# Kernel tuning notes

Measured on AMD Instinct MI355X. Metric: run time of the kernel, lower is better.

The kernel has to match this reference:

```python
import jax, jax.numpy as jnp
import numpy as np

N = 100000
E = 1600000
F_IN = 128
HID = 64
N_CLASS = 40
NEG_SLOPE = 0.2


def setup_inputs() -> dict:
    key = jax.random.key(0)
    ks = jax.random.split(key, 16)
    s = lambda *sh: 1.0 / np.sqrt(sh[0])
    inp = {
        "x": jax.random.normal(ks[0], (N, F_IN), dtype=jnp.float32),
        "edge_index": jax.random.randint(ks[1], (2, E), 0, N, dtype=jnp.int64),
        "W1": jax.random.normal(ks[2], (F_IN, HID), jnp.float32) * s(F_IN),
        "b1": jnp.zeros((HID,), jnp.float32),
        "Wc0": jax.random.normal(ks[3], (HID, HID), jnp.float32) * s(HID),
        "att_src0": jax.random.normal(ks[4], (HID,), jnp.float32) * s(HID),
        "att_dst0": jax.random.normal(ks[5], (HID,), jnp.float32) * s(HID),
        "bias0": jnp.zeros((HID,), jnp.float32),
        "Wc1": jax.random.normal(ks[6], (HID, HID), jnp.float32) * s(HID),
        "att_src1": jax.random.normal(ks[7], (HID,), jnp.float32) * s(HID),
        "att_dst1": jax.random.normal(ks[8], (HID,), jnp.float32) * s(HID),
        "bias1": jnp.zeros((HID,), jnp.float32),
        "W2": jax.random.normal(ks[9], (HID, N_CLASS), jnp.float32) * s(HID),
        "b2": jnp.zeros((N_CLASS,), jnp.float32),
    }
    return inp


def gat_conv(x, src, dst, W, att_src, att_dst, bias):
    # x: [N, Fin]; src/dst: [E'] (self-loops already appended)
    h = x @ W                                   # [N, Fout]
    a_s = h @ att_src                           # [N]
    a_d = h @ att_dst                           # [N]
    e = jax.nn.leaky_relu(a_s[src] + a_d[dst], NEG_SLOPE)   # [E']
    # segment softmax over edges grouped by destination node
    e_max = jax.ops.segment_max(e, dst, num_segments=N)     # every node has a self-loop
    ex = jnp.exp(e - e_max[dst])
    denom = jax.ops.segment_sum(ex, dst, num_segments=N)
    alpha = ex / (denom[dst] + 1e-16)                        # [E']
    out = jax.ops.segment_sum(h[src] * alpha[:, None], dst, num_segments=N)
    return out + bias


def reference(x, edge_index, W1, b1, Wc0, att_src0, att_dst0, bias0,
              Wc1, att_src1, att_dst1, bias1, W2, b2):
    # eval mode: dropout_adj and feature dropout are identity
    loop = jnp.arange(N, dtype=edge_index.dtype)
    src = jnp.concatenate([edge_index[0], loop])
    dst = jnp.concatenate([edge_index[1], loop])

    h = jax.nn.relu(x @ W1 + b1)
    h = gat_conv(h, src, dst, Wc0, att_src0, att_dst0, bias0)
    h = jax.nn.relu(h)
    h = gat_conv(h, src, dst, Wc1, att_src1, att_dst1, bias1)
    logits = h @ W2 + b2
    return jax.nn.log_softmax(logits, axis=-1)
```

## Files before the change

kernel.cpp:

```cpp
#include <hip/hip_runtime.h>

#define N_NODES 100000
#define N_EDGES 1600000
#define F_IN    128
#define HID     64
#define N_CLASS 40
#define NEG_SLOPE 0.2f
#define ET (N_EDGES + N_NODES)
#define ROW_BLOCKS ((N_NODES + 63) / 64)

#define NCB   7
#define CAP1  294912
#define BPC   144
#define NFB   782
#define CAPF  2624
#define NT1   ((ET + 2047) / 2048)

typedef __attribute__((ext_vector_type(8))) short bf16x8;
typedef __attribute__((ext_vector_type(4))) float f32x4;

__device__ __forceinline__ unsigned int f2bf(float f) {
    unsigned int u = __float_as_uint(f);
    return (u + 0x7fffu + ((u >> 16) & 1u)) >> 16;
}

__global__ __launch_bounds__(256) void k_prepw(const float* __restrict__ W1,
        const float* __restrict__ Wc0, const float* __restrict__ Wc1,
        const float* __restrict__ W2,
        unsigned short* __restrict__ Wt1, unsigned short* __restrict__ Wtc0,
        unsigned short* __restrict__ Wtc1, unsigned short* __restrict__ W2t,
        int* __restrict__ zbuf, int zcount) {
    int t = threadIdx.x;
    for (int i = t; i < zcount; i += 256) zbuf[i] = 0;
    for (int i = t; i < F_IN * HID; i += 256) {
        int k = i >> 6, n = i & 63;
        Wt1[n * F_IN + k] = (unsigned short)f2bf(W1[i]);
    }
    for (int i = t; i < HID * HID; i += 256) {
        int k = i >> 6, n = i & 63;
        Wtc0[n * HID + k] = (unsigned short)f2bf(Wc0[i]);
        Wtc1[n * HID + k] = (unsigned short)f2bf(Wc1[i]);
    }
    for (int i = t; i < 48 * HID; i += 256) {
        int n = i >> 6, k = i & 63;
        W2t[n * HID + k] = (n < N_CLASS)
            ? (unsigned short)f2bf(W2[k * N_CLASS + n]) : (unsigned short)0;
    }
}

__global__ __launch_bounds__(256) void k_lin1att(const float* __restrict__ x,
        const unsigned short* __restrict__ Wt1, const float* __restrict__ b1,
        const unsigned short* __restrict__ Wtc0,
        const float* __restrict__ att_s, const float* __restrict__ att_d,
        unsigned short* __restrict__ hb, float* __restrict__ as_,
        float* __restrict__ ad_) {
    __shared__ float xs[4][16 * 68];
    int t = threadIdx.x;
    int lane = t & 63, w = t >> 6;
    int quad = lane >> 4, lr = lane & 15;
    int rowg0 = blockIdx.x * 64 + w * 16;

    f32x4 zero = {0.f, 0.f, 0.f, 0.f};
    f32x4 acc[4] = {zero, zero, zero, zero};
    int arow = rowg0 + lr; if (arow >= N_NODES) arow = N_NODES - 1;
    const float* ab = x + (size_t)arow * F_IN;
    #pragma unroll
    for (int kc = 0; kc < 4; ++kc) {
        bf16x8 bw[4];
        #pragma unroll
        for (int nt = 0; nt < 4; ++nt)
            bw[nt] = *(const bf16x8*)(Wt1 + (nt * 16 + lr) * F_IN
                                      + kc * 32 + quad * 8);
        const float* ap = ab + kc * 32 + quad * 8;
        float4 a0 = *(const float4*)ap;
        float4 a1 = *(const float4*)(ap + 4);
        union { bf16x8 v; unsigned int u[4]; } af;
        af.u[0] = f2bf(a0.x) | (f2bf(a0.y) << 16);
        af.u[1] = f2bf(a0.z) | (f2bf(a0.w) << 16);
        af.u[2] = f2bf(a1.x) | (f2bf(a1.y) << 16);
        af.u[3] = f2bf(a1.z) | (f2bf(a1.w) << 16);
        #pragma unroll
        for (int nt = 0; nt < 4; ++nt)
            acc[nt] = __builtin_amdgcn_mfma_f32_16x16x32_bf16(
                          af.v, bw[nt], acc[nt], 0, 0, 0);
    }
    #pragma unroll
    for (int nt = 0; nt < 4; ++nt) {
        float bv = b1[nt * 16 + lr];
        #pragma unroll
        for (int reg = 0; reg < 4; ++reg)
            xs[w][(quad * 4 + reg) * 68 + nt * 16 + lr] =
                fmaxf(acc[nt][reg] + bv, 0.f);
    }
    f32x4 acc2[4] = {zero, zero, zero, zero};
    #pragma unroll
    for (int kc = 0; kc < 2; ++kc) {
        bf16x8 bw[4];
        #pragma unroll
        for (int nt = 0; nt < 4; ++nt)
            bw[nt] = *(const bf16x8*)(Wtc0 + (nt * 16 + lr) * HID
                                      + kc * 32 + quad * 8);
        const float* ap = xs[w] + lr * 68 + kc * 32 + quad * 8;
        float4 a0 = *(const float4*)ap;
        float4 a1 = *(const float4*)(ap + 4);
        union { bf16x8 v; unsigned int u[4]; } af;
        af.u[0] = f2bf(a0.x) | (f2bf(a0.y) << 16);
        af.u[1] = f2bf(a0.z) | (f2bf(a0.w) << 16);
        af.u[2] = f2bf(a1.x) | (f2bf(a1.y) << 16);
        af.u[3] = f2bf(a1.z) | (f2bf(a1.w) << 16);
        #pragma unroll
        for (int nt = 0; nt < 4; ++nt)
            acc2[nt] = __builtin_amdgcn_mfma_f32_16x16x32_bf16(
                          af.v, bw[nt], acc2[nt], 0, 0, 0);
    }
    float asv[4], adv[4];
    #pragma unroll
    for (int nt = 0; nt < 4; ++nt) {
        asv[nt] = att_s[nt * 16 + lr];
        adv[nt] = att_d[nt * 16 + lr];
    }
    #pragma unroll
    for (int reg = 0; reg < 4; ++reg) {
        float p1 = acc2[0][reg] * asv[0] + acc2[1][reg] * asv[1]
                 + acc2[2][reg] * asv[2] + acc2[3][reg] * asv[3];
        float p2 = acc2[0][reg] * adv[0] + acc2[1][reg] * adv[1]
                 + acc2[2][reg] * adv[2] + acc2[3][reg] * adv[3];
        #pragma unroll
        for (int off = 1; off < 16; off <<= 1) {
            p1 += __shfl_xor(p1, off, 64);
            p2 += __shfl_xor(p2, off, 64);
        }
        if (lr == 0) {
            int grow = rowg0 + quad * 4 + reg;
            if (grow < N_NODES) { as_[grow] = p1; ad_[grow] = p2; }
        }
    }
    #pragma unroll
    for (int nt = 0; nt < 4; ++nt)
        #pragma unroll
        for (int reg = 0; reg < 4; ++reg)
            xs[w][(quad * 4 + reg) * 68 + nt * 16 + lr] = acc2[nt][reg];
    #pragma unroll
    for (int j = 0; j < 2; ++j) {
        int task = j * 64 + lane;
        int r = task >> 3, g = task & 7;
        int grow = rowg0 + r;
        if (grow < N_NODES) {
            const float* p = xs[w] + r * 68 + g * 8;
            uint4 u;
            u.x = f2bf(p[0]) | (f2bf(p[1]) << 16);
            u.y = f2bf(p[2]) | (f2bf(p[3]) << 16);
            u.z = f2bf(p[4]) | (f2bf(p[5]) << 16);
            u.w = f2bf(p[6]) | (f2bf(p[7]) << 16);
            *(uint4*)(hb + (size_t)grow * HID + g * 8) = u;
        }
    }
}

__global__ __launch_bounds__(256) void k_gemm_att(
        const unsigned short* __restrict__ hin,
        const unsigned short* __restrict__ Wt,
        const float* __restrict__ att_s, const float* __restrict__ att_d,
        unsigned short* __restrict__ hb, float* __restrict__ as_,
        float* __restrict__ ad_) {
    __shared__ float xs[4][16 * 68];
    int t = threadIdx.x;
    int lane = t & 63, w = t >> 6;
    int quad = lane >> 4, lr = lane & 15;
    int rowg0 = blockIdx.x * 64 + w * 16;

    bf16x8 bfr[2][4];
    #pragma unroll
    for (int kc = 0; kc < 2; ++kc)
        #pragma unroll
        for (int nt = 0; nt < 4; ++nt)
            bfr[kc][nt] = *(const bf16x8*)(Wt + (nt * 16 + lr) * HID
                                           + kc * 32 + quad * 8);
    f32x4 zero = {0.f, 0.f, 0.f, 0.f};
    f32x4 acc[4] = {zero, zero, zero, zero};

    int arow = rowg0 + lr; if (arow >= N_NODES) arow = N_NODES - 1;
    #pragma unroll
    for (int kc = 0; kc < 2; ++kc) {
        bf16x8 af = *(const bf16x8*)(hin + (size_t)arow * HID
                                     + kc * 32 + quad * 8);
        #pragma unroll
        for (int nt = 0; nt < 4; ++nt)
            acc[nt] = __builtin_amdgcn_mfma_f32_16x16x32_bf16(
                          af, bfr[kc][nt], acc[nt], 0, 0, 0);
    }
    float asv[4], adv[4];
    #pragma unroll
    for (int nt = 0; nt < 4; ++nt) {
        asv[nt] = att_s[nt * 16 + lr];
        adv[nt] = att_d[nt * 16 + lr];
    }
    #pragma unroll
    for (int reg = 0; reg < 4; ++reg) {
        float p1 = acc[0][reg] * asv[0] + acc[1][reg] * asv[1]
                 + acc[2][reg] * asv[2] + acc[3][reg] * asv[3];
        float p2 = acc[0][reg] * adv[0] + acc[1][reg] * adv[1]
                 + acc[2][reg] * adv[2] + acc[3][reg] * adv[3];
        #pragma unroll
        for (int off = 1; off < 16; off <<= 1) {
            p1 += __shfl_xor(p1, off, 64);
            p2 += __shfl_xor(p2, off, 64);
        }
        if (lr == 0) {
            int grow = rowg0 + quad * 4 + reg;
            if (grow < N_NODES) { as_[grow] = p1; ad_[grow] = p2; }
        }
    }
    #pragma unroll
    for (int nt = 0; nt < 4; ++nt)
        #pragma unroll
        for (int reg = 0; reg < 4; ++reg)
            xs[w][(quad * 4 + reg) * 68 + nt * 16 + lr] = acc[nt][reg];
    #pragma unroll
    for (int j = 0; j < 2; ++j) {
        int task = j * 64 + lane;
        int r = task >> 3, g = task & 7;
        int grow = rowg0 + r;
        if (grow < N_NODES) {
            const float* p = xs[w] + r * 68 + g * 8;
            uint4 u;
            u.x = f2bf(p[0]) | (f2bf(p[1]) << 16);
            u.y = f2bf(p[2]) | (f2bf(p[3]) << 16);
            u.z = f2bf(p[4]) | (f2bf(p[5]) << 16);
            u.w = f2bf(p[6]) | (f2bf(p[7]) << 16);
            *(uint4*)(hb + (size_t)grow * HID + g * 8) = u;
        }
    }
}

__global__ __launch_bounds__(256) void k_part1(const int* __restrict__ ei,
        int* __restrict__ tail1, int2* __restrict__ buf1) {
    __shared__ int2 eb[2048];
    __shared__ int hist[NCB], lbase[NCB], loff[NCB], goff[NCB];
    int t = threadIdx.x;
    int tileBase = blockIdx.x * 2048;
    int total = ET - tileBase; if (total > 2048) total = 2048;
    if (t < NCB) hist[t] = 0;
    __syncthreads();

    int sr[8], dr[8];
    #pragma unroll
    for (int r = 0; r < 8; ++r) {
        int i = tileBase + r * 256 + t;
        int s = -1, d = -1;
        if (i < ET) {
            if (i < N_EDGES) { s = ei[i]; d = ei[N_EDGES + i]; }
            else             { s = d = i - N_EDGES; }
            atomicAdd(&hist[d >> 14], 1);
        }
        sr[r] = s; dr[r] = d;
    }
    __syncthreads();
    if (t == 0) {
        int run = 0;
        for (int b = 0; b < NCB; ++b) { lbase[b] = run; loff[b] = 0; run += hist[b]; }
    }
    __syncthreads();
    if (t < NCB && hist[t] > 0) goff[t] = atomicAdd(&tail1[t], hist[t]);
    #pragma unroll
    for (int r = 0; r < 8; ++r) {
        if (dr[r] >= 0) {
            int b = dr[r] >> 14;
            int p = lbase[b] + atomicAdd(&loff[b], 1);
            eb[p] = make_int2(sr[r], dr[r]);
        }
    }
    __syncthreads();
    for (int j = t; j < total; j += 256) {
        int2 e = eb[j];
        int b = e.y >> 14;
        buf1[(size_t)b * CAP1 + goff[b] + (j - lbase[b])] = e;
    }
}

__global__ __launch_bounds__(256) void k_part2(const int2* __restrict__ buf1,
        const int* __restrict__ tail1, int* __restrict__ fcnt,
        int2* __restrict__ buf2) {
    __shared__ int2 eb[2048];
    __shared__ int hist[128], lbase[128], loff[128], goff[128], sc[128];
    int t = threadIdx.x;
    int cb   = blockIdx.x / BPC;
    int tile = blockIdx.x % BPC;
    int n1 = tail1[cb];
    int base = tile * 2048;
    if (base >= n1) return;
    int total = n1 - base; if (total > 2048) total = 2048;
    if (t < 128) hist[t] = 0;
    __syncthreads();

    int sr[8], dr[8];
    #pragma unroll
    for (int r = 0; r < 8; ++r) {
        int i = base + r * 256 + t;
        int s = -1, d = -1;
        if (i < n1) {
            int2 e = buf1[(size_t)cb * CAP1 + i];
            s = e.x; d = e.y;
            atomicAdd(&hist[(d >> 7) & 127], 1);
        }
        sr[r] = s; dr[r] = d;
    }
    __syncthreads();
    if (t < 128) sc[t] = hist[t];
    __syncthreads();
    for (int off = 1; off < 128; off <<= 1) {
        int u = (t < 128 && t >= off) ? sc[t - off] : 0;
        __syncthreads();
        if (t < 128) sc[t] += u;
        __syncthreads();
    }
    if (t < 128) { lbase[t] = sc[t] - hist[t]; loff[t] = 0; }
    __syncthreads();
    if (t < 128 && hist[t] > 0)
        goff[t] = atomicAdd(&fcnt[cb * 128 + t], hist[t]);
    #pragma unroll
    for (int r = 0; r < 8; ++r) {
        if (dr[r] >= 0) {
            int f = (dr[r] >> 7) & 127;
            int p = lbase[f] + atomicAdd(&loff[f], 1);
            eb[p] = make_int2(sr[r], dr[r]);
        }
    }
    __syncthreads();
    for (int j = t; j < total; j += 256) {
        int2 e = eb[j];
        int f = (e.y >> 7) & 127;
        buf2[(size_t)(e.y >> 7) * CAPF + goff[f] + (j - lbase[f])] = e;
    }
}

__global__ __launch_bounds__(1024) void k_fscan(const int* __restrict__ fcnt,
        int* __restrict__ fbase, int* __restrict__ rowptr) {
    __shared__ int s[1024];
    int t = threadIdx.x;
    int v = (t < NFB) ? fcnt[t] : 0;
    s[t] = v;
    __syncthreads();
    for (int off = 1; off < 1024; off <<= 1) {
        int u = (t >= off) ? s[t - off] : 0;
        __syncthreads();
        s[t] += u;
        __syncthreads();
    }
    if (t < NFB) fbase[t] = s[t] - v;
    if (t == 0) rowptr[N_NODES] = ET;
}

__global__ __launch_bounds__(256) void k_part3(const int2* __restrict__ buf2,
        const int* __restrict__ fcnt, const int* __restrict__ fbase,
        int* __restrict__ rowptr, int* __restrict__ col,
        int* __restrict__ dhistg) {
    __shared__ int2 eb[CAPF];
    __shared__ int cs[CAPF];
    __shared__ int hist[128], lbase[128], loff[128], sc[128], dh[64];
    int t = threadIdx.x;
    int fb = blockIdx.x;
    int nF = fcnt[fb];
    int gb = fbase[fb];
    int nbase = fb * 128;
    if (t < 128) hist[t] = 0;
    if (t >= 128 && t < 192) dh[t - 128] = 0;
    __syncthreads();
    for (int j = t; j < nF; j += 256) {
        int2 e = buf2[(size_t)fb * CAPF + j];
        eb[j] = e;
        atomicAdd(&hist[e.y - nbase], 1);
    }
    __syncthreads();
    if (t < 128) sc[t] = hist[t];
    __syncthreads();
    for (int off = 1; off < 128; off <<= 1) {
        int u = (t < 128 && t >= off) ? sc[t - off] : 0;
        __syncthreads();
        if (t < 128) sc[t] += u;
        __syncthreads();
    }
    if (t < 128) { lbase[t] = sc[t] - hist[t]; loff[t] = 0; }
    __syncthreads();
    if (t < 128 && nbase + t < N_NODES) {
        rowptr[nbase + t] = gb + lbase[t];
        int dg = hist[t]; if (dg > 63) dg = 63;
        atomicAdd(&dh[dg], 1);
    }
    for (int j = t; j < nF; j += 256) {
        int2 e = eb[j];
        int r = e.y - nbase;
        int p = lbase[r] + atomicAdd(&loff[r], 1);
        cs[p] = e.x;
    }
    __syncthreads();
    for (int j = t; j < nF; j += 256) col[gb + j] = cs[j];
    if (t < 64 && dh[t] > 0) atomicAdd(&dhistg[t], dh[t]);
}

__global__ __launch_bounds__(64) void k_dscan(const int* __restrict__ dhist,
        int* __restrict__ dbase) {
    int t = threadIdx.x;
    int v = dhist[t];
    int s = v;
    #pragma unroll
    for (int off = 1; off < 64; off <<= 1) {
        int u = __shfl_up(s, off, 64);
        if (t >= off) s += u;
    }
    dbase[t] = s - v;
}

__global__ __launch_bounds__(256) void k_dscatter(const int* __restrict__ rowptr,
        int* __restrict__ dbase, int* __restrict__ nodeord) {
    __shared__ int lh[64], goff[64];
    int t = threadIdx.x;
    if (t < 64) lh[t] = 0;
    __syncthreads();
    int i = blockIdx.x * 256 + t;
    int deg = -1, lrank = 0;
    if (i < N_NODES) {
        deg = rowptr[i + 1] - rowptr[i];
        if (deg > 63) deg = 63;
        lrank = atomicAdd(&lh[deg], 1);
    }
    __syncthreads();
    if (t < 64) goff[t] = (lh[t] > 0) ? atomicAdd(&dbase[t], lh[t]) : 0;
    __syncthreads();
    if (deg >= 0) nodeord[goff[deg] + lrank] = i;
}

template <bool RELU>
__global__ __launch_bounds__(256) void k_gat_agg(const int* __restrict__ rowptr,
        const int* __restrict__ col, const unsigned short* __restrict__ hb,
        const float* __restrict__ as_, const float* __restrict__ ad_,
        const float* __restrict__ bias, const int* __restrict__ nodeord,
        unsigned short* __restrict__ outb) {
    int t = threadIdx.x;
    int lane = t & 63;
    int wid = blockIdx.x * 4 + (t >> 6);
    int l8 = lane & 7;
    int ch = l8 * 8;
    int d = nodeord[wid * 8 + (lane >> 3)];
    int beg = rowptr[d];
    int deg = rowptr[d + 1] - beg;
    float add = ad_[d];
    int degw = deg;
    degw = max(degw, __shfl_xor(degw, 8, 64));
    degw = max(degw, __shfl_xor(degw, 16, 64));
    degw = max(degw, __shfl_xor(degw, 32, 64));

    float a0=0.f,a1=0.f,a2=0.f,a3=0.f,a4=0.f,a5=0.f,a6=0.f,a7=0.f,den=0.f;
    const unsigned short* hch = hb + ch;
    for (int c = 0; c < degw; c += 8) {
        int idx = c + l8;
        int sj = 0; float wj = 0.f;
        if (idx < deg) {
            sj = col[beg + idx];
            float e = as_[sj] + add;
            e = (e > 0.f) ? e : NEG_SLOPE * e;
            wj = __expf(e);
        }
        #pragma unroll
        for (int j = 0; j < 8; ++j) {
            int sl = (lane & 56) | j;
            int   s  = __shfl(sj, sl, 64);
            float w0 = __shfl(wj, sl, 64);
            den += w0;
            uint4 hv = *(const uint4*)(hch + (size_t)s * HID);
            a0 = fmaf(w0, __uint_as_float(hv.x << 16),         a0);
            a1 = fmaf(w0, __uint_as_float(hv.x & 0xffff0000u), a1);
            a2 = fmaf(w0, __uint_as_float(hv.y << 16),         a2);
            a3 = fmaf(w0, __uint_as_float(hv.y & 0xffff0000u), a3);
            a4 = fmaf(w0, __uint_as_float(hv.z << 16),         a4);
            a5 = fmaf(w0, __uint_as_float(hv.z & 0xffff0000u), a5);
            a6 = fmaf(w0, __uint_as_float(hv.w << 16),         a6);
            a7 = fmaf(w0, __uint_as_float(hv.w & 0xffff0000u), a7);
        }
    }
    float inv = 1.f / (den + 1e-16f);
    float4 bA = *(const float4*)(bias + ch);
    float4 bB = *(const float4*)(bias + ch + 4);
    float o0 = fmaf(a0, inv, bA.x), o1 = fmaf(a1, inv, bA.y);
    float o2 = fmaf(a2, inv, bA.z), o3 = fmaf(a3, inv, bA.w);
    float o4 = fmaf(a4, inv, bB.x), o5 = fmaf(a5, inv, bB.y);
    float o6 = fmaf(a6, inv, bB.z), o7 = fmaf(a7, inv, bB.w);
    if (RELU) {
        o0 = fmaxf(o0, 0.f); o1 = fmaxf(o1, 0.f);
        o2 = fmaxf(o2, 0.f); o3 = fmaxf(o3, 0.f);
        o4 = fmaxf(o4, 0.f); o5 = fmaxf(o5, 0.f);
        o6 = fmaxf(o6, 0.f); o7 = fmaxf(o7, 0.f);
    }
    uint4 u;
    u.x = f2bf(o0) | (f2bf(o1) << 16);
    u.y = f2bf(o2) | (f2bf(o3) << 16);
    u.z = f2bf(o4) | (f2bf(o5) << 16);
    u.w = f2bf(o6) | (f2bf(o7) << 16);
    *(uint4*)(outb + (size_t)d * HID + ch) = u;
}

__global__ __launch_bounds__(256) void k_final(
        const unsigned short* __restrict__ aggb,
        const unsigned short* __restrict__ W2t, const float* __restrict__ b2,
        float* __restrict__ out) {
    __shared__ float xs[64 * 44];
    int t = threadIdx.x;
    int lane = t & 63, w = t >> 6;
    int quad = lane >> 4, lr = lane & 15;
    int rowg0 = blockIdx.x * 64 + w * 16;
    int base = blockIdx.x * 64;
    int rem = N_NODES - base; if (rem > 64) rem = 64;

    bf16x8 bfr[2][3];
    #pragma unroll
    for (int kc = 0; kc < 2; ++kc)
        #pragma unroll
        for (int nt = 0; nt < 3; ++nt)
            bfr[kc][nt] = *(const bf16x8*)(W2t + (nt * 16 + lr) * HID
                                           + kc * 32 + quad * 8);
    f32x4 zero = {0.f, 0.f, 0.f, 0.f};
    f32x4 acc[3] = {zero, zero, zero};
    int arow = rowg0 + lr; if (arow >= N_NODES) arow = N_NODES - 1;
    #pragma unroll
    for (int kc = 0; kc < 2; ++kc) {
        bf16x8 af = *(const bf16x8*)(aggb + (size_t)arow * HID
                                     + kc * 32 + quad * 8);
        #pragma unroll
        for (int nt = 0; nt < 3; ++nt)
            acc[nt] = __builtin_amdgcn_mfma_f32_16x16x32_bf16(
                          af, bfr[kc][nt], acc[nt], 0, 0, 0);
    }
    float bc[3];
    #pragma unroll
    for (int nt = 0; nt < 3; ++nt) {
        int cl = nt * 16 + lr;
        bc[nt] = (cl < N_CLASS) ? b2[cl] : -1e30f;
    }
    #pragma unroll
    for (int reg = 0; reg < 4; ++reg) {
        float v0 = acc[0][reg] + bc[0];
        float v1 = acc[1][reg] + bc[1];
        float v2 = acc[2][reg] + bc[2];
        float m = fmaxf(fmaxf(v0, v1), v2);
        #pragma unroll
        for (int off = 1; off < 16; off <<= 1)
            m = fmaxf(m, __shfl_xor(m, off, 64));
        float ss = __expf(v0 - m) + __expf(v1 - m) + __expf(v2 - m);
        #pragma unroll
        for (int off = 1; off < 16; off <<= 1)
            ss += __shfl_xor(ss, off, 64);
        float lse = m + logf(ss);
        int r = w * 16 + quad * 4 + reg;
        xs[r * 44 + lr]      = v0 - lse;
        xs[r * 44 + 16 + lr] = v1 - lse;
        if (lr < 8) xs[r * 44 + 32 + lr] = v2 - lse;
    }
    __syncthreads();
    #pragma unroll
    for (int j = 0; j < 3; ++j) {
        int idx = j * 256 + t;
        if (idx < rem * 10) {
            int r = idx / 10, c4 = idx - r * 10;
            float4 v = *(const float4*)(xs + r * 44 + c4 * 4);
            *(float4*)(out + (size_t)base * N_CLASS + idx * 4) = v;
        }
    }
}

extern "C" void kernel_launch(void* const* d_in, const int* in_sizes, int n_in,
                              void* d_out, int out_size, void* d_ws, size_t ws_size,
                              hipStream_t stream) {
    const float* x     = (const float*)d_in[0];
    const int*   ei    = (const int*)  d_in[1];
    const float* W1    = (const float*)d_in[2];
    const float* b1    = (const float*)d_in[3];
    const float* Wc0   = (const float*)d_in[4];
    const float* as0   = (const float*)d_in[5];
    const float* ad0   = (const float*)d_in[6];
    const float* bias0 = (const float*)d_in[7];
    const float* Wc1   = (const float*)d_in[8];
    const float* as1   = (const float*)d_in[9];
    const float* ad1   = (const float*)d_in[10];
    const float* bias1 = (const float*)d_in[11];
    const float* W2    = (const float*)d_in[12];
    const float* b2    = (const float*)d_in[13];
    float* out = (float*)d_out;

    char* basep = (char*)d_ws;
    char* R1 = basep;
    char* R2 = basep + (size_t)N_NODES * HID * 4;
    unsigned short* agg1b = (unsigned short*)R1;
    int*            nodeord = (int*)(R1 + (size_t)N_NODES * HID * 2);
    int2*           buf2  = (int2*)R1;
    unsigned short* hb    = (unsigned short*)R2;
    unsigned short* agg0b = (unsigned short*)(R2 + (size_t)N_NODES * HID * 2);
    int2*           buf1  = (int2*)R2;

    char* mp = R2 + (size_t)N_NODES * HID * 4;
    unsigned short* Wt1  = (unsigned short*)mp;  mp += F_IN * HID * 2;
    unsigned short* Wtc0 = (unsigned short*)mp;  mp += HID * HID * 2;
    unsigned short* Wtc1 = (unsigned short*)mp;  mp += HID * HID * 2;
    unsigned short* W2t  = (unsigned short*)mp;  mp += 48 * HID * 2;
    float* as_   = (float*)mp;                   mp += N_NODES * 4;
    float* ad_   = (float*)mp;                   mp += N_NODES * 4;
    int*   col   = (int*)mp;                     mp += (size_t)ET * 4;
    int*   tail1 = (int*)mp;                     mp += NCB * 4;
    int*   fcnt  = (int*)mp;                     mp += NFB * 4;
    int*   fbase = (int*)mp;                     mp += NFB * 4;
    int*   dhist = (int*)mp;                     mp += 64 * 4;
    int*   dbase = (int*)mp;                     mp += 64 * 4;
    int*   rowptr= (int*)mp;
    const int ZCOUNT = NCB + 2 * NFB + 128;

    const int AGG_BLOCKS = N_NODES / 32;
    const int NODE_BLOCKS = (N_NODES + 255) / 256;

    k_prepw<<<1, 256, 0, stream>>>(W1, Wc0, Wc1, W2, Wt1, Wtc0, Wtc1, W2t,
                                   tail1, ZCOUNT);
    k_part1<<<NT1, 256, 0, stream>>>(ei, tail1, buf1);
    k_part2<<<NCB * BPC, 256, 0, stream>>>(buf1, tail1, fcnt, buf2);
    k_fscan<<<1, 1024, 0, stream>>>(fcnt, fbase, rowptr);
    k_part3<<<NFB, 256, 0, stream>>>(buf2, fcnt, fbase, rowptr, col, dhist);
    k_dscan<<<1, 64, 0, stream>>>(dhist, dbase);
    k_dscatter<<<NODE_BLOCKS, 256, 0, stream>>>(rowptr, dbase, nodeord);

    k_lin1att<<<ROW_BLOCKS, 256, 0, stream>>>(x, Wt1, b1, Wtc0, as0, ad0,
                                              hb, as_, ad_);
    k_gat_agg<true><<<AGG_BLOCKS, 256, 0, stream>>>(
        rowptr, col, hb, as_, ad_, bias0, nodeord, agg0b);

    k_gemm_att<<<ROW_BLOCKS, 256, 0, stream>>>(agg0b, Wtc1, as1, ad1,
                                               hb, as_, ad_);
    k_gat_agg<false><<<AGG_BLOCKS, 256, 0, stream>>>(
        rowptr, col, hb, as_, ad_, bias1, nodeord, agg1b);

    k_final<<<ROW_BLOCKS, 256, 0, stream>>>(agg1b, W2t, b2, out);
}
```

Measured before the change: 312.9 us.

## Fuse edge partition pass with first linear layer and fold scans into last blocks

Merges the first edge-partition pass and the input linear/attention kernel into one launch, with blocks split by index, so the two independent stages can overlap on the GPU. Edge records are packed into 32-bit words (source shifted left, low destination bits) instead of int2 pairs, halving the partition buffer traffic. The separate single-block scan kernels are removed: the last-finishing block of part2 and part3, detected with an atomic counter, does the scan. The weight prep kernel now runs on 32 blocks, and the workspace layout is reorganized, adding completion counters and some risk from the packed-index bit widths.

```diff
diff --git a/kernel.cpp b/kernel.cpp
--- a/kernel.cpp
+++ b/kernel.cpp
@@ -30,27 +30,378 @@
         unsigned short* __restrict__ Wt1, unsigned short* __restrict__ Wtc0,
         unsigned short* __restrict__ Wtc1, unsigned short* __restrict__ W2t,
         int* __restrict__ zbuf, int zcount) {
-    int t = threadIdx.x;
-    for (int i = t; i < zcount; i += 256) zbuf[i] = 0;
-    for (int i = t; i < F_IN * HID; i += 256) {
+    int g = blockIdx.x * 256 + threadIdx.x;
+    int stride = gridDim.x * 256;
+    for (int i = g; i < zcount; i += stride) zbuf[i] = 0;
+    for (int i = g; i < F_IN * HID; i += stride) {
         int k = i >> 6, n = i & 63;
         Wt1[n * F_IN + k] = (unsigned short)f2bf(W1[i]);
     }
-    for (int i = t; i < HID * HID; i += 256) {
+    for (int i = g; i < HID * HID; i += stride) {
         int k = i >> 6, n = i & 63;
         Wtc0[n * HID + k] = (unsigned short)f2bf(Wc0[i]);
         Wtc1[n * HID + k] = (unsigned short)f2bf(Wc1[i]);
     }
-    for (int i = t; i < 48 * HID; i += 256) {
+    for (int i = g; i < 48 * HID; i += stride) {
         int n = i >> 6, k = i & 63;
         W2t[n * HID + k] = (n < N_CLASS)
             ? (unsigned short)f2bf(W2[k * N_CLASS + n]) : (unsigned short)0;
     }
 }
 
-__global__ __launch_bounds__(256) void k_lin1att(const float* __restrict__ x,
-        const unsigned short* __restrict__ Wt1, const float* __restrict__ b1,
-        const unsigned short* __restrict__ Wtc0,
+__global__ __launch_bounds__(256) void k_p1lin(
+        const int* __restrict__ ei, int* __restrict__ tail1,
+        unsigned int* __restrict__ buf1,
+        const float* __restrict__ x, const unsigned short* __restrict__ Wt1,
+        const float* __restrict__ b1, const unsigned short* __restrict__ Wtc0,
+        const float* __restrict__ att_s, const float* __restrict__ att_d,
+        unsigned short* __restrict__ hb, float* __restrict__ as_,
+        float* __restrict__ ad_) {
+    __shared__ __align__(16) char smem[17408];
+    __shared__ int hist[NCB], lb[NCB], cbase[NCB];
+    int t = threadIdx.x;
+    int lane = t & 63, w = t >> 6;
+
+    if (blockIdx.x < NT1) {
+        unsigned int* eb = (unsigned int*)smem;
+        int tileBase = blockIdx.x * 2048;
+        int total = ET - tileBase; if (total > 2048) total = 2048;
+        if (t < NCB) hist[t] = 0;
+        __syncthreads();
+        unsigned long long ltm = (1ull << lane) - 1ull;
+        unsigned int pk[8]; int ps[8];
+        #pragma unroll
+        for (int r = 0; r < 8; ++r) {
+            int i = tileBase + r * 256 + t;
+            int s = 0, d = 0;
+            bool valid = (i < ET);
+            if (valid) {
+                if (i < N_EDGES) { s = ei[i]; d = ei[N_EDGES + i]; }
+                else             { s = d = i - N_EDGES; }
+            }
+            int b = valid ? (d >> 14) : -1;
+            unsigned long long m[NCB];
+            #pragma unroll
+            for (int q = 0; q < NCB; ++q) m[q] = __ballot(b == q);
+            int cnt = 0;
+            #pragma unroll
+            for (int q = 0; q < NCB; ++q) if (lane == q) cnt = __popcll(m[q]);
+            int old = 0;
+            if (lane < NCB) old = atomicAdd(&hist[lane], cnt);
+            int bsafe = valid ? b : 0;
+            int basew = __shfl(old, bsafe, 64);
+            if (valid) {
+                int rank = 0;
+                #pragma unroll
+                for (int q = 0; q < NCB; ++q)
+                    if (b == q) rank = (int)__popcll(m[q] & ltm);
+                pk[r] = ((unsigned int)s << 14) | ((unsigned int)d & 16383u);
+                ps[r] = (basew + rank) | (b << 12);
+            } else ps[r] = -1;
+        }
+        __syncthreads();
+        if (t == 0) {
+            int run = 0;
+            #pragma unroll
+            for (int q = 0; q < NCB; ++q) { int h = hist[q]; lb[q] = run; run += h; }
+        }
+        __syncthreads();
+        if (t < NCB) {
+            int g = (hist[t] > 0) ? atomicAdd(&tail1[t], hist[t]) : 0;
+            cbase[t] = g - lb[t];
+        }
+        #pragma unroll
+        for (int r = 0; r < 8; ++r) {
+            if (ps[r] >= 0) {
+                int b = ps[r] >> 12, pos = ps[r] & 4095;
+                eb[lb[b] + pos] = pk[r];
+            }
+        }
+        __syncthreads();
+        int B1 = lb[1], B2 = lb[2], B3 = lb[3], B4 = lb[4], B5 = lb[5], B6 = lb[6];
+        for (int j = t; j < total; j += 256) {
+            unsigned int p = eb[j];
+            int b = (j >= B1) + (j >= B2) + (j >= B3) + (j >= B4)
+                  + (j >= B5) + (j >= B6);
+            buf1[(size_t)b * CAP1 + cbase[b] + j] = p;
+        }
+    } else {
+        int quad = lane >> 4, lr = lane & 15;
+        int rowg0 = (int)(blockIdx.x - NT1) * 64 + w * 16;
+        float* xs = (float*)smem + w * (16 * 68);
+
+        f32x4 zero = {0.f, 0.f, 0.f, 0.f};
+        f32x4 acc[4] = {zero, zero, zero, zero};
+        int arow = rowg0 + lr; if (arow >= N_NODES) arow = N_NODES - 1;
+        const float* ab = x + (size_t)arow * F_IN;
+        #pragma unroll
+        for (int kc = 0; kc < 4; ++kc) {
+            bf16x8 bw[4];
+            #pragma unroll
+            for (int nt = 0; nt < 4; ++nt)
+                bw[nt] = *(const bf16x8*)(Wt1 + (nt * 16 + lr) * F_IN
+                                          + kc * 32 + quad * 8);
+            const float* ap = ab + kc * 32 + quad * 8;
+            float4 a0 = *(const float4*)ap;
+            float4 a1 = *(const float4*)(ap + 4);
+            union { bf16x8 v; unsigned int u[4]; } af;
+            af.u[0] = f2bf(a0.x) | (f2bf(a0.y) << 16);
+            af.u[1] = f2bf(a0.z) | (f2bf(a0.w) << 16);
+            af.u[2] = f2bf(a1.x) | (f2bf(a1.y) << 16);
+            af.u[3] = f2bf(a1.z) | (f2bf(a1.w) << 16);
+            #pragma unroll
+            for (int nt = 0; nt < 4; ++nt)
+                acc[nt] = __builtin_amdgcn_mfma_f32_16x16x32_bf16(
+                              af.v, bw[nt], acc[nt], 0, 0, 0);
+        }
+        #pragma unroll
+        for (int nt = 0; nt < 4; ++nt) {
+            float bv = b1[nt * 16 + lr];
+            #pragma unroll
+            for (int reg = 0; reg < 4; ++reg)
+                xs[(quad * 4 + reg) * 68 + nt * 16 + lr] =
+                    fmaxf(acc[nt][reg] + bv, 0.f);
+        }
+        f32x4 acc2[4] = {zero, zero, zero, zero};
+        #pragma unroll
+        for (int kc = 0; kc < 2; ++kc) {
+            bf16x8 bw[4];
+            #pragma unroll
+            for (int nt = 0; nt < 4; ++nt)
+                bw[nt] = *(const bf16x8*)(Wtc0 + (nt * 16 + lr) * HID
+                                          + kc * 32 + quad * 8);
+            const float* ap = xs + lr * 68 + kc * 32 + quad * 8;
+            float4 a0 = *(const float4*)ap;
+            float4 a1 = *(const float4*)(ap + 4);
+            union { bf16x8 v; unsigned int u[4]; } af;
+            af.u[0] = f2bf(a0.x) | (f2bf(a0.y) << 16);
+            af.u[1] = f2bf(a0.z) | (f2bf(a0.w) << 16);
+            af.u[2] = f2bf(a1.x) | (f2bf(a1.y) << 16);
+            af.u[3] = f2bf(a1.z) | (f2bf(a1.w) << 16);
+            #pragma unroll
+            for (int nt = 0; nt < 4; ++nt)
+                acc2[nt] = __builtin_amdgcn_mfma_f32_16x16x32_bf16(
+                              af.v, bw[nt], acc2[nt], 0, 0, 0);
+        }
+        float asv[4], adv[4];
+        #pragma unroll
+        for (int nt = 0; nt < 4; ++nt) {
+            asv[nt] = att_s[nt * 16 + lr];
+            adv[nt] = att_d[nt * 16 + lr];
+        }
+        #pragma unroll
+        for (int reg = 0; reg < 4; ++reg) {
+            float p1 = acc2[0][reg] * asv[0] + acc2[1][reg] * asv[1]
+                     + acc2[2][reg] * asv[2] + acc2[3][reg] * asv[3];
+            float p2 = acc2[0][reg] * adv[0] + acc2[1][reg] * adv[1]
+                     + acc2[2][reg] * adv[2] + acc2[3][reg] * adv[3];
+            #pragma unroll
+            for (int off = 1; off < 16; off <<= 1) {
+                p1 += __shfl_xor(p1, off, 64);
+                p2 += __shfl_xor(p2, off, 64);
+            }
+            if (lr == 0) {
+                int grow = rowg0 + quad * 4 + reg;
+                if (grow < N_NODES) { as_[grow] = p1; ad_[grow] = p2; }
+            }
+        }
+        #pragma unroll
+        for (int nt = 0; nt < 4; ++nt)
+            #pragma unroll
+            for (int reg = 0; reg < 4; ++reg)
+                xs[(quad * 4 + reg) * 68 + nt * 16 + lr] = acc2[nt][reg];
+        #pragma unroll
+        for (int j = 0; j < 2; ++j) {
+            int task = j * 64 + lane;
+            int r = task >> 3, g = task & 7;
+            int grow = rowg0 + r;
+            if (grow < N_NODES) {
+                const float* p = xs + r * 68 + g * 8;
+                uint4 u;
+                u.x = f2bf(p[0]) | (f2bf(p[1]) << 16);
+                u.y = f2bf(p[2]) | (f2bf(p[3]) << 16);
+                u.z = f2bf(p[4]) | (f2bf(p[5]) << 16);
+                u.w = f2bf(p[6]) | (f2bf(p[7]) << 16);
+                *(uint4*)(hb + (size_t)grow * HID + g * 8) = u;
+            }
+        }
+    }
+}
+
+__global__ __launch_bounds__(256) void k_part2(const unsigned int* __restrict__ buf1,
+        const int* __restrict__ tail1, int* __restrict__ fcnt,
+        unsigned int* __restrict__ buf2, int* __restrict__ fbase,
+        int* __restrict__ rowptr, int* __restrict__ done0) {
+    __shared__ unsigned int eb[2048];
+    __shared__ int hist[128], lbase[128], loff[128], goff[128], sc[128];
+    __shared__ int lastflag, wsum4[4];
+    int t = threadIdx.x;
+    int cb   = blockIdx.x / BPC;
+    int tile = blockIdx.x % BPC;
+    int n1 = tail1[cb];
+    int base = tile * 2048;
+    if (base < n1) {
+        int total = n1 - base; if (total > 2048) total = 2048;
+        if (t < 128) hist[t] = 0;
+        __syncthreads();
+        unsigned int pr[8]; int fr[8];
+        #pragma unroll
+        for (int r = 0; r < 8; ++r) {
+            int i = base + r * 256 + t;
+            int f = -1; unsigned int p = 0;
+            if (i < n1) {
+                p = buf1[(size_t)cb * CAP1 + i];
+                f = (int)((p >> 7) & 127u);
+                atomicAdd(&hist[f], 1);
+            }
+            pr[r] = p; fr[r] = f;
+        }
+        __syncthreads();
+        if (t < 128) sc[t] = hist[t];
+        __syncthreads();
+        for (int off = 1; off < 128; off <<= 1) {
+            int u = (t < 128 && t >= off) ? sc[t - off] : 0;
+            __syncthreads();
+            if (t < 128) sc[t] += u;
+            __syncthreads();
+        }
+        if (t < 128) { lbase[t] = sc[t] - hist[t]; loff[t] = 0; }
+        __syncthreads();
+        if (t < 128 && hist[t] > 0)
+            goff[t] = atomicAdd(&fcnt[cb * 128 + t], hist[t]);
+        #pragma unroll
+        for (int r = 0; r < 8; ++r) {
+            if (fr[r] >= 0) {
+                int f = fr[r];
+                int pos = lbase[f] + atomicAdd(&loff[f], 1);
+                eb[pos] = (pr[r] & 127u) | ((pr[r] >> 14) << 7)
+                        | ((unsigned int)f << 24);
+            }
+        }
+        __syncthreads();
+        for (int j = t; j < total; j += 256) {
+            unsigned int q = eb[j];
+            int f = (int)(q >> 24);
+            buf2[(size_t)(cb * 128 + f) * CAPF + goff[f] + (j - lbase[f])] =
+                q & 0xFFFFFFu;
+        }
+    }
+    if (t == 0) lastflag = (atomicAdd(done0, 1) == NCB * BPC - 1);
+    __syncthreads();
+    if (lastflag) {
+        __threadfence();
+        int k0 = t * 4;
+        int v0 = (k0     < NFB) ? fcnt[k0]     : 0;
+        int v1 = (k0 + 1 < NFB) ? fcnt[k0 + 1] : 0;
+        int v2 = (k0 + 2 < NFB) ? fcnt[k0 + 2] : 0;
+        int v3 = (k0 + 3 < NFB) ? fcnt[k0 + 3] : 0;
+        int s1 = v0 + v1, s2 = s1 + v2, s3 = s2 + v3;
+        int lane = t & 63, w = t >> 6;
+        int ws = s3;
+        #pragma unroll
+        for (int off = 1; off < 64; off <<= 1) {
+            int u = __shfl_up(ws, off, 64);
+            if (lane >= off) ws += u;
+        }
+        if (lane == 63) wsum4[w] = ws;
+        __syncthreads();
+        int wb = 0;
+        #pragma unroll
+        for (int q = 0; q < 4; ++q) if (q < w) wb += wsum4[q];
+        int ex = wb + ws - s3;
+        if (k0     < NFB) fbase[k0]     = ex;
+        if (k0 + 1 < NFB) fbase[k0 + 1] = ex + v0;
+        if (k0 + 2 < NFB) fbase[k0 + 2] = ex + s1;
+        if (k0 + 3 < NFB) fbase[k0 + 3] = ex + s2;
+        if (t == 0) rowptr[N_NODES] = ET;
+    }
+}
+
+__global__ __launch_bounds__(256) void k_part3(const unsigned int* __restrict__ buf2,
+        const int* __restrict__ fcnt, const int* __restrict__ fbase,
+        int* __restrict__ rowptr, int* __restrict__ col,
+        int* __restrict__ dhistg, int* __restrict__ dbase,
+        int* __restrict__ done1) {
+    __shared__ unsigned int eb[CAPF];
+    __shared__ int cs[CAPF];
+    __shared__ int hist[128], lbase[128], loff[128], sc[128], dh[64];
+    __shared__ int lastflag;
+    int t = threadIdx.x;
+    int fb = blockIdx.x;
+    int nF = fcnt[fb];
+    int gb = fbase[fb];
+    int nbase = fb * 128;
+    if (t < 128) hist[t] = 0;
+    if (t >= 128 && t < 192) dh[t - 128] = 0;
+    __syncthreads();
+    for (int j = t; j < nF; j += 256) {
+        unsigned int q = buf2[(size_t)fb * CAPF + j];
+        eb[j] = q;
+        atomicAdd(&hist[q & 127u], 1);
+    }
+    __syncthreads();
+    if (t < 128) sc[t] = hist[t];
+    __syncthreads();
+    for (int off = 1; off < 128; off <<= 1) {
+        int u = (t < 128 && t >= off) ? sc[t - off] : 0;
+        __syncthreads();
+        if (t < 128) sc[t] += u;
+        __syncthreads();
+    }
+    if (t < 128) { lbase[t] = sc[t] - hist[t]; loff[t] = 0; }
+    __syncthreads();
+    if (t < 128 && nbase + t < N_NODES) {
+        rowptr[nbase + t] = gb + lbase[t];
+        int dg = hist[t]; if (dg > 63) dg = 63;
+        atomicAdd(&dh[dg], 1);
+    }
+    for (int j = t; j < nF; j += 256) {
+        unsigned int q = eb[j];
+        int r = (int)(q & 127u);
+        int p = lbase[r] + atomicAdd(&loff[r], 1);
+        cs[p] = (int)(q >> 7);
+    }
+    __syncthreads();
+    for (int j = t; j < nF; j += 256) col[gb + j] = cs[j];
+    if (t < 64 && dh[t] > 0) atomicAdd(&dhistg[t], dh[t]);
+    __syncthreads();
+    if (t == 0) lastflag = (atomicAdd(done1, 1) == NFB - 1);
+    __syncthreads();
+    if (lastflag && t < 64) {
+        __threadfence();
+        int v = dhistg[t];
+        int s = v;
+        #pragma unroll
+        for (int off = 1; off < 64; off <<= 1) {
+            int u = __shfl_up(s, off, 64);
+            if (t >= off) s += u;
+        }
+        dbase[t] = s - v;
+    }
+}
+
+__global__ __launch_bounds__(256) void k_dscatter(const int* __restrict__ rowptr,
+        int* __restrict__ dbase, int* __restrict__ nodeord) {
+    __shared__ int lh[64], goff[64];
+    int t = threadIdx.x;
+    if (t < 64) lh[t] = 0;
+    __syncthreads();
+    int i = blockIdx.x * 256 + t;
+    int deg = -1, lrank = 0;
+    if (i < N_NODES) {
+        deg = rowptr[i + 1] - rowptr[i];
+        if (deg > 63) deg = 63;
+        lrank = atomicAdd(&lh[deg], 1);
+    }
+    __syncthreads();
+    if (t < 64) goff[t] = (lh[t] > 0) ? atomicAdd(&dbase[t], lh[t]) : 0;
+    __syncthreads();
+    if (deg >= 0) nodeord[goff[deg] + lrank] = i;
+}
+
+__global__ __launch_bounds__(256) void k_gemm_att(
+        const unsigned short* __restrict__ hin,
+        const unsigned short* __restrict__ Wt,
         const float* __restrict__ att_s, const float* __restrict__ att_d,
         unsigned short* __restrict__ hb, float* __restrict__ as_,
         float* __restrict__ ad_) {
@@ -60,58 +411,25 @@
     int quad = lane >> 4, lr = lane & 15;
     int rowg0 = blockIdx.x * 64 + w * 16;
 
+    bf16x8 bfr[2][4];
+    #pragma unroll
+    for (int kc = 0; kc < 2; ++kc)
+        #pragma unroll
+        for (int nt = 0; nt < 4; ++nt)
+            bfr[kc][nt] = *(const bf16x8*)(Wt + (nt * 16 + lr) * HID
+                                           + kc * 32 + quad * 8);
     f32x4 zero = {0.f, 0.f, 0.f, 0.f};
     f32x4 acc[4] = {zero, zero, zero, zero};
+
     int arow = rowg0 + lr; if (arow >= N_NODES) arow = N_NODES - 1;
-    const float* ab = x + (size_t)arow * F_IN;
-    #pragma unroll
-    for (int kc = 0; kc < 4; ++kc) {
-        bf16x8 bw[4];
-        #pragma unroll
-        for (int nt = 0; nt < 4; ++nt)
-            bw[nt] = *(const bf16x8*)(Wt1 + (nt * 16 + lr) * F_IN
-                                      + kc * 32 + quad * 8);
-        const float* ap = ab + kc * 32 + quad * 8;
-        float4 a0 = *(const float4*)ap;
-        float4 a1 = *(const float4*)(ap + 4);
-        union { bf16x8 v; unsigned int u[4]; } af;
-        af.u[0] = f2bf(a0.x) | (f2bf(a0.y) << 16);
-        af.u[1] = f2bf(a0.z) | (f2bf(a0.w) << 16);
-        af.u[2] = f2bf(a1.x) | (f2bf(a1.y) << 16);
-        af.u[3] = f2bf(a1.z) | (f2bf(a1.w) << 16);
+    #pragma unroll
+    for (int kc = 0; kc < 2; ++kc) {
+        bf16x8 af = *(const bf16x8*)(hin + (size_t)arow * HID
+                                     + kc * 32 + quad * 8);
         #pragma unroll
         for (int nt = 0; nt < 4; ++nt)
             acc[nt] = __builtin_amdgcn_mfma_f32_16x16x32_bf16(
-                          af.v, bw[nt], acc[nt], 0, 0, 0);
-    }
-    #pragma unroll
-    for (int nt = 0; nt < 4; ++nt) {
-        float bv = b1[nt * 16 + lr];
-        #pragma unroll
-        for (int reg = 0; reg < 4; ++reg)
-            xs[w][(quad * 4 + reg) * 68 + nt * 16 + lr] =
-                fmaxf(acc[nt][reg] + bv, 0.f);
-    }
-    f32x4 acc2[4] = {zero, zero, zero, zero};
-    #pragma unroll
-    for (int kc = 0; kc < 2; ++kc) {
-        bf16x8 bw[4];
-        #pragma unroll
-        for (int nt = 0; nt < 4; ++nt)
-            bw[nt] = *(const bf16x8*)(Wtc0 + (nt * 16 + lr) * HID
-                                      + kc * 32 + quad * 8);
-        const float* ap = xs[w] + lr * 68 + kc * 32 + quad * 8;
-        float4 a0 = *(const float4*)ap;
-        float4 a1 = *(const float4*)(ap + 4);
-        union { bf16x8 v; unsigned int u[4]; } af;
-        af.u[0] = f2bf(a0.x) | (f2bf(a0.y) << 16);
-        af.u[1] = f2bf(a0.z) | (f2bf(a0.w) << 16);
-        af.u[2] = f2bf(a1.x) | (f2bf(a1.y) << 16);
-        af.u[3] = f2bf(a1.z) | (f2bf(a1.w) << 16);
-        #pragma unroll
-        for (int nt = 0; nt < 4; ++nt)
-            acc2[nt] = __builtin_amdgcn_mfma_f32_16x16x32_bf16(
-                          af.v, bw[nt], acc2[nt], 0, 0, 0);
+                          af, bfr[kc][nt], acc[nt], 0, 0, 0);
     }
     float asv[4], adv[4];
     #pragma unroll
@@ -121,10 +439,10 @@
     }
     #pragma unroll
     for (int reg = 0; reg < 4; ++reg) {
-        float p1 = acc2[0][reg] * asv[0] + acc2[1][reg] * asv[1]
-                 + acc2[2][reg] * asv[2] + acc2[3][reg] * asv[3];
-        float p2 = acc2[0][reg] * adv[0] + acc2[1][reg] * adv[1]
-                 + acc2[2][reg] * adv[2] + acc2[3][reg] * adv[3];
+        float p1 = acc[0][reg] * asv[0] + acc[1][reg] * asv[1]
+                 + acc[2][reg] * asv[2] + acc[3][reg] * asv[3];
+        float p2 = acc[0][reg] * adv[0] + acc[1][reg] * adv[1]
+                 + acc[2][reg] * adv[2] + acc[3][reg] * adv[3];
         #pragma unroll
         for (int off = 1; off < 16; off <<= 1) {
             p1 += __shfl_xor(p1, off, 64);
@@ -139,7 +457,7 @@
     for (int nt = 0; nt < 4; ++nt)
         #pragma unroll
         for (int reg = 0; reg < 4; ++reg)
-            xs[w][(quad * 4 + reg) * 68 + nt * 16 + lr] = acc2[nt][reg];
+            xs[w][(quad * 4 + reg) * 68 + nt * 16 + lr] = acc[nt][reg];
     #pragma unroll
     for (int j = 0; j < 2; ++j) {
         int task = j * 64 + lane;
@@ -155,279 +473,6 @@
             *(uint4*)(hb + (size_t)grow * HID + g * 8) = u;
         }
     }
-}
-
-__global__ __launch_bounds__(256) void k_gemm_att(
-        const unsigned short* __restrict__ hin,
-        const unsigned short* __restrict__ Wt,
-        const float* __restrict__ att_s, const float* __restrict__ att_d,
-        unsigned short* __restrict__ hb, float* __restrict__ as_,
-        float* __restrict__ ad_) {
-    __shared__ float xs[4][16 * 68];
-    int t = threadIdx.x;
-    int lane = t & 63, w = t >> 6;
-    int quad = lane >> 4, lr = lane & 15;
-    int rowg0 = blockIdx.x * 64 + w * 16;
-
-    bf16x8 bfr[2][4];
-    #pragma unroll
-    for (int kc = 0; kc < 2; ++kc)
-        #pragma unroll
-        for (int nt = 0; nt < 4; ++nt)
-            bfr[kc][nt] = *(const bf16x8*)(Wt + (nt * 16 + lr) * HID
-                                           + kc * 32 + quad * 8);
-    f32x4 zero = {0.f, 0.f, 0.f, 0.f};
-    f32x4 acc[4] = {zero, zero, zero, zero};
-
-    int arow = rowg0 + lr; if (arow >= N_NODES) arow = N_NODES - 1;
-    #pragma unroll
-    for (int kc = 0; kc < 2; ++kc) {
-        bf16x8 af = *(const bf16x8*)(hin + (size_t)arow * HID
-                                     + kc * 32 + quad * 8);
-        #pragma unroll
-        for (int nt = 0; nt < 4; ++nt)
-            acc[nt] = __builtin_amdgcn_mfma_f32_16x16x32_bf16(
-                          af, bfr[kc][nt], acc[nt], 0, 0, 0);
-    }
-    float asv[4], adv[4];
-    #pragma unroll
-    for (int nt = 0; nt < 4; ++nt) {
-        asv[nt] = att_s[nt * 16 + lr];
-        adv[nt] = att_d[nt * 16 + lr];
-    }
-    #pragma unroll
-    for (int reg = 0; reg < 4; ++reg) {
-        float p1 = acc[0][reg] * asv[0] + acc[1][reg] * asv[1]
-                 + acc[2][reg] * asv[2] + acc[3][reg] * asv[3];
-        float p2 = acc[0][reg] * adv[0] + acc[1][reg] * adv[1]
-                 + acc[2][reg] * adv[2] + acc[3][reg] * adv[3];
-        #pragma unroll
-        for (int off = 1; off < 16; off <<= 1) {
-            p1 += __shfl_xor(p1, off, 64);
-            p2 += __shfl_xor(p2, off, 64);
-        }
-        if (lr == 0) {
-            int grow = rowg0 + quad * 4 + reg;
-            if (grow < N_NODES) { as_[grow] = p1; ad_[grow] = p2; }
-        }
-    }
-    #pragma unroll
-    for (int nt = 0; nt < 4; ++nt)
-        #pragma unroll
-        for (int reg = 0; reg < 4; ++reg)
-            xs[w][(quad * 4 + reg) * 68 + nt * 16 + lr] = acc[nt][reg];
-    #pragma unroll
-    for (int j = 0; j < 2; ++j) {
-        int task = j * 64 + lane;
-        int r = task >> 3, g = task & 7;
-        int grow = rowg0 + r;
-        if (grow < N_NODES) {
-            const float* p = xs[w] + r * 68 + g * 8;
-            uint4 u;
-            u.x = f2bf(p[0]) | (f2bf(p[1]) << 16);
-            u.y = f2bf(p[2]) | (f2bf(p[3]) << 16);
-            u.z = f2bf(p[4]) | (f2bf(p[5]) << 16);
-            u.w = f2bf(p[6]) | (f2bf(p[7]) << 16);
-            *(uint4*)(hb + (size_t)grow * HID + g * 8) = u;
-        }
-    }
-}
-
-__global__ __launch_bounds__(256) void k_part1(const int* __restrict__ ei,
-        int* __restrict__ tail1, int2* __restrict__ buf1) {
-    __shared__ int2 eb[2048];
-    __shared__ int hist[NCB], lbase[NCB], loff[NCB], goff[NCB];
-    int t = threadIdx.x;
-    int tileBase = blockIdx.x * 2048;
-    int total = ET - tileBase; if (total > 2048) total = 2048;
-    if (t < NCB) hist[t] = 0;
-    __syncthreads();
-
-    int sr[8], dr[8];
-    #pragma unroll
-    for (int r = 0; r < 8; ++r) {
-        int i = tileBase + r * 256 + t;
-        int s = -1, d = -1;
-        if (i < ET) {
-            if (i < N_EDGES) { s = ei[i]; d = ei[N_EDGES + i]; }
-            else             { s = d = i - N_EDGES; }
-            atomicAdd(&hist[d >> 14], 1);
-        }
-        sr[r] = s; dr[r] = d;
-    }
-    __syncthreads();
-    if (t == 0) {
-        int run = 0;
-        for (int b = 0; b < NCB; ++b) { lbase[b] = run; loff[b] = 0; run += hist[b]; }
-    }
-    __syncthreads();
-    if (t < NCB && hist[t] > 0) goff[t] = atomicAdd(&tail1[t], hist[t]);
-    #pragma unroll
-    for (int r = 0; r < 8; ++r) {
-        if (dr[r] >= 0) {
-            int b = dr[r] >> 14;
-            int p = lbase[b] + atomicAdd(&loff[b], 1);
-            eb[p] = make_int2(sr[r], dr[r]);
-        }
-    }
-    __syncthreads();
-    for (int j = t; j < total; j += 256) {
-        int2 e = eb[j];
-        int b = e.y >> 14;
-        buf1[(size_t)b * CAP1 + goff[b] + (j - lbase[b])] = e;
-    }
-}
-
-__global__ __launch_bounds__(256) void k_part2(const int2* __restrict__ buf1,
-        const int* __restrict__ tail1, int* __restrict__ fcnt,
-        int2* __restrict__ buf2) {
-    __shared__ int2 eb[2048];
-    __shared__ int hist[128], lbase[128], loff[128], goff[128], sc[128];
-    int t = threadIdx.x;
-    int cb   = blockIdx.x / BPC;
-    int tile = blockIdx.x % BPC;
-    int n1 = tail1[cb];
-    int base = tile * 2048;
-    if (base >= n1) return;
-    int total = n1 - base; if (total > 2048) total = 2048;
-    if (t < 128) hist[t] = 0;
-    __syncthreads();
-
-    int sr[8], dr[8];
-    #pragma unroll
-    for (int r = 0; r < 8; ++r) {
-        int i = base + r * 256 + t;
-        int s = -1, d = -1;
-        if (i < n1) {
-            int2 e = buf1[(size_t)cb * CAP1 + i];
-            s = e.x; d = e.y;
-            atomicAdd(&hist[(d >> 7) & 127], 1);
-        }
-        sr[r] = s; dr[r] = d;
-    }
-    __syncthreads();
-    if (t < 128) sc[t] = hist[t];
-    __syncthreads();
-    for (int off = 1; off < 128; off <<= 1) {
-        int u = (t < 128 && t >= off) ? sc[t - off] : 0;
-        __syncthreads();
-        if (t < 128) sc[t] += u;
-        __syncthreads();
-    }
-    if (t < 128) { lbase[t] = sc[t] - hist[t]; loff[t] = 0; }
-    __syncthreads();
-    if (t < 128 && hist[t] > 0)
-        goff[t] = atomicAdd(&fcnt[cb * 128 + t], hist[t]);
-    #pragma unroll
-    for (int r = 0; r < 8; ++r) {
-        if (dr[r] >= 0) {
-            int f = (dr[r] >> 7) & 127;
-            int p = lbase[f] + atomicAdd(&loff[f], 1);
-            eb[p] = make_int2(sr[r], dr[r]);
-        }
-    }
-    __syncthreads();
-    for (int j = t; j < total; j += 256) {
-        int2 e = eb[j];
-        int f = (e.y >> 7) & 127;
-        buf2[(size_t)(e.y >> 7) * CAPF + goff[f] + (j - lbase[f])] = e;
-    }
-}
-
-__global__ __launch_bounds__(1024) void k_fscan(const int* __restrict__ fcnt,
-        int* __restrict__ fbase, int* __restrict__ rowptr) {
-    __shared__ int s[1024];
-    int t = threadIdx.x;
-    int v = (t < NFB) ? fcnt[t] : 0;
-    s[t] = v;
-    __syncthreads();
-    for (int off = 1; off < 1024; off <<= 1) {
-        int u = (t >= off) ? s[t - off] : 0;
-        __syncthreads();
-        s[t] += u;
-        __syncthreads();
-    }
-    if (t < NFB) fbase[t] = s[t] - v;
-    if (t == 0) rowptr[N_NODES] = ET;
-}
-
-__global__ __launch_bounds__(256) void k_part3(const int2* __restrict__ buf2,
-        const int* __restrict__ fcnt, const int* __restrict__ fbase,
-        int* __restrict__ rowptr, int* __restrict__ col,
-        int* __restrict__ dhistg) {
-    __shared__ int2 eb[CAPF];
-    __shared__ int cs[CAPF];
-    __shared__ int hist[128], lbase[128], loff[128], sc[128], dh[64];
-    int t = threadIdx.x;
-    int fb = blockIdx.x;
-    int nF = fcnt[fb];
-    int gb = fbase[fb];
-    int nbase = fb * 128;
-    if (t < 128) hist[t] = 0;
-    if (t >= 128 && t < 192) dh[t - 128] = 0;
-    __syncthreads();
-    for (int j = t; j < nF; j += 256) {
-        int2 e = buf2[(size_t)fb * CAPF + j];
-        eb[j] = e;
-        atomicAdd(&hist[e.y - nbase], 1);
-    }
-    __syncthreads();
-    if (t < 128) sc[t] = hist[t];
-    __syncthreads();
-    for (int off = 1; off < 128; off <<= 1) {
-        int u = (t < 128 && t >= off) ? sc[t - off] : 0;
-        __syncthreads();
-        if (t < 128) sc[t] += u;
-        __syncthreads();
-    }
-    if (t < 128) { lbase[t] = sc[t] - hist[t]; loff[t] = 0; }
-    __syncthreads();
-    if (t < 128 && nbase + t < N_NODES) {
-        rowptr[nbase + t] = gb + lbase[t];
-        int dg = hist[t]; if (dg > 63) dg = 63;
-        atomicAdd(&dh[dg], 1);
-    }
-    for (int j = t; j < nF; j += 256) {
-        int2 e = eb[j];
-        int r = e.y - nbase;
-        int p = lbase[r] + atomicAdd(&loff[r], 1);
-        cs[p] = e.x;
-    }
-    __syncthreads();
-    for (int j = t; j < nF; j += 256) col[gb + j] = cs[j];
-    if (t < 64 && dh[t] > 0) atomicAdd(&dhistg[t], dh[t]);
-}
-
-__global__ __launch_bounds__(64) void k_dscan(const int* __restrict__ dhist,
-        int* __restrict__ dbase) {
-    int t = threadIdx.x;
-    int v = dhist[t];
-    int s = v;
-    #pragma unroll
-    for (int off = 1; off < 64; off <<= 1) {
-        int u = __shfl_up(s, off, 64);
-        if (t >= off) s += u;
-    }
-    dbase[t] = s - v;
-}
-
-__global__ __launch_bounds__(256) void k_dscatter(const int* __restrict__ rowptr,
-        int* __restrict__ dbase, int* __restrict__ nodeord) {
-    __shared__ int lh[64], goff[64];
-    int t = threadIdx.x;
-    if (t < 64) lh[t] = 0;
-    __syncthreads();
-    int i = blockIdx.x * 256 + t;
-    int deg = -1, lrank = 0;
-    if (i < N_NODES) {
-        deg = rowptr[i + 1] - rowptr[i];
-        if (deg > 63) deg = 63;
-        lrank = atomicAdd(&lh[deg], 1);
-    }
-    __syncthreads();
-    if (t < 64) goff[t] = (lh[t] > 0) ? atomicAdd(&dbase[t], lh[t]) : 0;
-    __syncthreads();
-    if (deg >= 0) nodeord[goff[deg] + lrank] = i;
 }
 
 template <bool RELU>
@@ -586,46 +631,45 @@
     const float* b2    = (const float*)d_in[13];
     float* out = (float*)d_out;
 
-    char* basep = (char*)d_ws;
-    char* R1 = basep;
-    char* R2 = basep + (size_t)N_NODES * HID * 4;
-    unsigned short* agg1b = (unsigned short*)R1;
-    int*            nodeord = (int*)(R1 + (size_t)N_NODES * HID * 2);
-    int2*           buf2  = (int2*)R1;
-    unsigned short* hb    = (unsigned short*)R2;
-    unsigned short* agg0b = (unsigned short*)(R2 + (size_t)N_NODES * HID * 2);
-    int2*           buf1  = (int2*)R2;
-
-    char* mp = R2 + (size_t)N_NODES * HID * 4;
-    unsigned short* Wt1  = (unsigned short*)mp;  mp += F_IN * HID * 2;
-    unsigned short* Wtc0 = (unsigned short*)mp;  mp += HID * HID * 2;
-    unsigned short* Wtc1 = (unsigned short*)mp;  mp += HID * HID * 2;
-    unsigned short* W2t  = (unsigned short*)mp;  mp += 48 * HID * 2;
-    float* as_   = (float*)mp;                   mp += N_NODES * 4;
-    float* ad_   = (float*)mp;                   mp += N_NODES * 4;
-    int*   col   = (int*)mp;                     mp += (size_t)ET * 4;
-    int*   tail1 = (int*)mp;                     mp += NCB * 4;
-    int*   fcnt  = (int*)mp;                     mp += NFB * 4;
-    int*   fbase = (int*)mp;                     mp += NFB * 4;
-    int*   dhist = (int*)mp;                     mp += 64 * 4;
-    int*   dbase = (int*)mp;                     mp += 64 * 4;
-    int*   rowptr= (int*)mp;
-    const int ZCOUNT = NCB + 2 * NFB + 128;
-
-    const int AGG_BLOCKS = N_NODES / 32;
+    char* p = (char*)d_ws;
+    unsigned short* hb    = (unsigned short*)p; p += (size_t)N_NODES * HID * 2;
+    unsigned short* agg0b = (unsigned short*)p; p += (size_t)N_NODES * HID * 2;
+    char* pbuf = p;
+    unsigned int*   buf1  = (unsigned int*)pbuf;
+    unsigned int*   buf2  = (unsigned int*)(pbuf + (size_t)NCB * CAP1 * 4);
+    unsigned short* agg1b = (unsigned short*)pbuf;
+    p += (size_t)NCB * CAP1 * 4 + (size_t)NFB * CAPF * 4;
+    int* col = (int*)p;                          p += (size_t)ET * 4;
+    unsigned short* Wt1  = (unsigned short*)p;   p += F_IN * HID * 2;
+    unsigned short* Wtc0 = (unsigned short*)p;   p += HID * HID * 2;
+    unsigned short* Wtc1 = (unsigned short*)p;   p += HID * HID * 2;
+    unsigned short* W2t  = (unsigned short*)p;   p += 48 * HID * 2;
+    float* as_ = (float*)p;                      p += (size_t)N_NODES * 4;
+    float* ad_ = (float*)p;                      p += (size_t)N_NODES * 4;
+    int* tail1 = (int*)p;
+    int* fcnt  = tail1 + NCB;
+    int* fbase = fcnt + NFB;
+    int* dhist = fbase + NFB;
+    int* dbase = dhist + 64;
+    int* done  = dbase + 64;
+    const int ZCOUNT = NCB + 2 * NFB + 128 + 2;
+    p += (size_t)ZCOUNT * 4;
+    int* rowptr  = (int*)p;                      p += (size_t)(N_NODES + 1) * 4;
+    int* nodeord = (int*)p;
+
+    const int AGG_BLOCKS  = N_NODES / 32;
     const int NODE_BLOCKS = (N_NODES + 255) / 256;
 
-    k_prepw<<<1, 256, 0, stream>>>(W1, Wc0, Wc1, W2, Wt1, Wtc0, Wtc1, W2t,
-                                   tail1, ZCOUNT);
-    k_part1<<<NT1, 256, 0, stream>>>(ei, tail1, buf1);
-    k_part2<<<NCB * BPC, 256, 0, stream>>>(buf1, tail1, fcnt, buf2);
-    k_fscan<<<1, 1024, 0, stream>>>(fcnt, fbase, rowptr);
-    k_part3<<<NFB, 256, 0, stream>>>(buf2, fcnt, fbase, rowptr, col, dhist);
-    k_dscan<<<1, 64, 0, stream>>>(dhist, dbase);
+    k_prepw<<<32, 256, 0, stream>>>(W1, Wc0, Wc1, W2, Wt1, Wtc0, Wtc1, W2t,
+                                    tail1, ZCOUNT);
+    k_p1lin<<<NT1 + ROW_BLOCKS, 256, 0, stream>>>(
+        ei, tail1, buf1, x, Wt1, b1, Wtc0, as0, ad0, hb, as_, ad_);
+    k_part2<<<NCB * BPC, 256, 0, stream>>>(buf1, tail1, fcnt, buf2, fbase,
+                                           rowptr, done + 0);
+    k_part3<<<NFB, 256, 0, stream>>>(buf2, fcnt, fbase, rowptr, col, dhist,
+                                     dbase, done + 1);
     k_dscatter<<<NODE_BLOCKS, 256, 0, stream>>>(rowptr, dbase, nodeord);
 
-    k_lin1att<<<ROW_BLOCKS, 256, 0, stream>>>(x, Wt1, b1, Wtc0, as0, ad0,
-                                              hb, as_, ad_);
     k_gat_agg<true><<<AGG_BLOCKS, 256, 0, stream>>>(
         rowptr, col, hb, as_, ad_, bias0, nodeord, agg0b);
 
```

New measurement: 293.2 us. 6.3% less time.
